# Kernel optimization log

Hardware: AMD Instinct MI355X
Metric: run time of the kernel (lower is better)

Reference implementation:

```python
import jax, jax.numpy as jnp
import numpy as np

B, TM1, E, D = 512, 256, 256, 256  # batch, T-1, encoder_hidden, decoder_hidden


def setup_inputs() -> dict:
    key = jax.random.key(0)
    ks = jax.random.split(key, 10)
    s = 0.05
    return {
        "input_encoded": jax.random.normal(ks[0], (B, TM1, E), dtype=jnp.float32),
        "y_history": jax.random.normal(ks[1], (B, TM1, 1), dtype=jnp.float32),
        # attn_layer: Linear(2D+E -> E), Tanh, Linear(E -> 1)
        "attn_w1": jax.random.normal(ks[2], (E, 2 * D + E), dtype=jnp.float32) * s,
        "attn_b1": jnp.zeros((E,), jnp.float32),
        "attn_w2": jax.random.normal(ks[3], (1, E), dtype=jnp.float32) * s,
        "attn_b2": jnp.zeros((1,), jnp.float32),
        # LSTM cell: input_size=1, hidden=D
        "W_ih": jax.random.normal(ks[4], (4 * D, 1), dtype=jnp.float32) * s,
        "W_hh": jax.random.normal(ks[5], (4 * D, D), dtype=jnp.float32) * s,
        "b_ih": jnp.zeros((4 * D,), jnp.float32),
        "b_hh": jnp.zeros((4 * D,), jnp.float32),
        # fc: Linear(E+1 -> 1), weight init normal_()
        "fc_w": jax.random.normal(ks[6], (1, E + 1), dtype=jnp.float32),
        "fc_b": jnp.zeros((1,), jnp.float32),
        # fc_final: Linear(D+E -> 2) (probabilistic)
        "fcf_w": jax.random.normal(ks[7], (2, D + E), dtype=jnp.float32) * s,
        "fcf_b": jnp.zeros((2,), jnp.float32),
    }


def _forward(input_encoded, y_history, attn_w1, attn_b1, attn_w2, attn_b2,
             W_ih, W_hh, b_ih, b_hh, fc_w, fc_b, fcf_w, fcf_b):
    # Split attn first linear into [hidden|cell] part and encoder part.
    w1_hc = attn_w1[:, : 2 * D]   # (E, 2D)
    w1_enc = attn_w1[:, 2 * D:]   # (E, E)
    # Encoder projection is invariant across timesteps: compute once. (B,TM1,E)
    enc_proj = jnp.einsum("bte,fe->btf", input_encoded, w1_enc) + attn_b1

    def step(carry, y_t):
        h, c, _ = carry  # h,c: (B,D); y_t: (B,1)
        hc = jnp.concatenate([h, c], axis=1)                     # (B, 2D)
        pre = jnp.tanh(enc_proj + (hc @ w1_hc.T)[:, None, :])    # (B, TM1, E)
        scores = jnp.einsum("bte,oe->bto", pre, attn_w2)[..., 0] + attn_b2[0]  # (B, TM1)
        alpha = jax.nn.softmax(scores, axis=1)
        context = jnp.einsum("bt,bte->be", alpha, input_encoded)  # (B, E)
        y_tilde = jnp.concatenate([context, y_t], axis=1) @ fc_w.T + fc_b  # (B,1)
        # LSTM cell (torch gate order: i, f, g, o)
        gates = y_tilde @ W_ih.T + b_ih + h @ W_hh.T + b_hh  # (B, 4D)
        i, f, g, o = jnp.split(gates, 4, axis=1)
        i = jax.nn.sigmoid(i); f = jax.nn.sigmoid(f)
        g = jnp.tanh(g); o = jax.nn.sigmoid(o)
        c_new = f * c + i * g
        h_new = o * jnp.tanh(c_new)
        return (h_new, c_new, context), None

    h0 = jnp.zeros((input_encoded.shape[0], D), input_encoded.dtype)
    c0 = jnp.zeros_like(h0)
    ctx0 = jnp.zeros((input_encoded.shape[0], E), input_encoded.dtype)
    ys = jnp.transpose(y_history, (1, 0, 2))  # (TM1, B, 1)
    (h, c, context), _ = jax.lax.scan(step, (h0, c0, ctx0), ys)
    return jnp.concatenate([h, context], axis=1) @ fcf_w.T + fcf_b  # (B, 2)


def reference(input_encoded, y_history, attn_w1, attn_b1, attn_w2, attn_b2,
              W_ih, W_hh, b_ih, b_hh, fc_w, fc_b, fcf_w, fcf_b):
    return _forward(input_encoded, y_history, attn_w1, attn_b1, attn_w2, attn_b2,
                    W_ih, W_hh, b_ih, b_hh, fc_w, fc_b, fcf_w, fcf_b)
```

## Files before the change

### kernel.cpp

```cpp
#include <hip/hip_runtime.h>
#include <cstdint>
#include <cstddef>


typedef _Float16 half8 __attribute__((ext_vector_type(8)));
typedef _Float16 half4v __attribute__((ext_vector_type(4)));
typedef _Float16 half2v __attribute__((ext_vector_type(2)));

__device__ __forceinline__ float rcpf_(float x) { return __builtin_amdgcn_rcpf(x); }
__device__ __forceinline__ float sigmoidf_(float x) { return rcpf_(1.f + __expf(-x)); }
__device__ __forceinline__ float tanhf_(float x) { return 1.f - 2.f * rcpf_(1.f + __expf(2.f * x)); }

#if defined(__has_builtin)
#if __has_builtin(__builtin_amdgcn_fdot2)
#define HAS_FDOT2 1
#endif
#endif
#ifndef HAS_FDOT2
#define HAS_FDOT2 0
#endif

__device__ __forceinline__ float fdot2_(half2v a, half2v b, float c) {
#if HAS_FDOT2
  return __builtin_amdgcn_fdot2(a, b, c, false);
#else
  return fmaf((float)a[0], (float)b[0], fmaf((float)a[1], (float)b[1], c));
#endif
}

__device__ __forceinline__ float dot8_(half8 w, half8 h, float acc) {
  acc = fdot2_(__builtin_shufflevector(w, w, 0, 1), __builtin_shufflevector(h, h, 0, 1), acc);
  acc = fdot2_(__builtin_shufflevector(w, w, 2, 3), __builtin_shufflevector(h, h, 2, 3), acc);
  acc = fdot2_(__builtin_shufflevector(w, w, 4, 5), __builtin_shufflevector(h, h, 4, 5), acc);
  acc = fdot2_(__builtin_shufflevector(w, w, 6, 7), __builtin_shufflevector(h, h, 6, 7), acc);
  return acc;
}


__global__ void k_prep_wT(const float* __restrict__ w1, float* __restrict__ wT) {
  int id = blockIdx.x * 256 + threadIdx.x;
  int e = id >> 8, f = id & 255;
  wT[id] = w1[f * 768 + 512 + e];
}

__global__ void k_prep_xh(const float* __restrict__ x, _Float16* __restrict__ xh) {
  int id = blockIdx.x * 256 + threadIdx.x;
  float4 v = reinterpret_cast<const float4*>(x)[id];
  half4v h;
  h[0] = (_Float16)v.x; h[1] = (_Float16)v.y; h[2] = (_Float16)v.z; h[3] = (_Float16)v.w;
  reinterpret_cast<half4v*>(xh)[id] = h;
}

__global__ void k_prep_w1hcQ(const float* __restrict__ w1, _Float16* __restrict__ o) {
  int id = blockIdx.x * 256 + threadIdx.x;
  int m = id & 7, lane = (id >> 3) & 511, c = id >> 12;
  int e = lane >> 1, kh = lane & 1;
  o[id] = (_Float16)w1[e * 768 + kh * 256 + c * 8 + m];
}

__global__ void k_prep_whhG(const float* __restrict__ whh, _Float16* __restrict__ o) {
  int id = blockIdx.x * 256 + threadIdx.x;
  int m = id & 7, j = (id >> 3) & 1023, c = id >> 13;
  o[id] = (_Float16)whh[j * 256 + c * 8 + m];
}

__global__ __launch_bounds__(256) void k_xf(const float* __restrict__ x,
                                            const float* __restrict__ fcw,
                                            float* __restrict__ xf) {
  __shared__ float xl[16][256];
  __shared__ float fw[256];
  __shared__ float part[16][17];
  const int tid = threadIdx.x;
  const int m0 = blockIdx.x * 16;
  fw[tid] = fcw[tid];
#pragma unroll
  for (int r = 0; r < 16; ++r) xl[r][tid] = x[(size_t)(m0 + r) * 256 + tid];
  __syncthreads();
  int r = tid >> 4, p = tid & 15;
  float s = 0.f;
#pragma unroll
  for (int u = 0; u < 16; ++u) s = fmaf(xl[r][p * 16 + u], fw[p * 16 + u], s);
  part[r][p] = s;
  __syncthreads();
  if (tid < 16) {
    float t = 0.f;
#pragma unroll
    for (int p2 = 0; p2 < 16; ++p2) t += part[tid][p2];
    xf[m0 + tid] = t;
  }
}

__global__ __launch_bounds__(256) void k_encp(const float* __restrict__ x,
                                              const float* __restrict__ wT,
                                              const float* __restrict__ b1,
                                              _Float16* __restrict__ Ph2) {
  __shared__ __align__(16) float xl[16][256];
  const int tid = threadIdx.x;
  const int m0 = blockIdx.x * 16;
#pragma unroll
  for (int r = 0; r < 16; ++r) xl[r][tid] = x[(size_t)(m0 + r) * 256 + tid];
  __syncthreads();
  float acc[16];
#pragma unroll
  for (int r = 0; r < 16; ++r) acc[r] = 0.f;
  for (int e = 0; e < 256; e += 4) {
    float w0 = wT[(e + 0) * 256 + tid];
    float w1_ = wT[(e + 1) * 256 + tid];
    float w2_ = wT[(e + 2) * 256 + tid];
    float w3_ = wT[(e + 3) * 256 + tid];
#pragma unroll
    for (int r = 0; r < 16; ++r) {
      float4 xv = *reinterpret_cast<const float4*>(&xl[r][e]);
      acc[r] = fmaf(xv.x, w0, acc[r]);
      acc[r] = fmaf(xv.y, w1_, acc[r]);
      acc[r] = fmaf(xv.z, w2_, acc[r]);
      acc[r] = fmaf(xv.w, w3_, acc[r]);
    }
  }
  float bb = b1[tid];
  const int e = tid;
#pragma unroll
  for (int r = 0; r < 16; ++r) {
    int m = m0 + r, b = m >> 8, t = m & 255;
    float p = __expf(2.f * (acc[r] + bb));
    Ph2[((size_t)(b * 32 + (e >> 3)) * 256 + t) * 8 + (e & 7)] = (_Float16)p;
  }
}

#define SC1(pv, c) { \
  float4 qa = q4[2*(c)], wa = w4[2*(c)]; \
  sacc0 = fmaf(wa.x, rcpf_(fmaf((float)pv[0], qa.x, 1.f)), sacc0); \
  sacc1 = fmaf(wa.y, rcpf_(fmaf((float)pv[1], qa.y, 1.f)), sacc1); \
  sacc0 = fmaf(wa.z, rcpf_(fmaf((float)pv[2], qa.z, 1.f)), sacc0); \
  sacc1 = fmaf(wa.w, rcpf_(fmaf((float)pv[3], qa.w, 1.f)), sacc1); \
  float4 qb = q4[2*(c)+1], wb = w4[2*(c)+1]; \
  sacc0 = fmaf(wb.x, rcpf_(fmaf((float)pv[4], qb.x, 1.f)), sacc0); \
  sacc1 = fmaf(wb.y, rcpf_(fmaf((float)pv[5], qb.y, 1.f)), sacc1); \
  sacc0 = fmaf(wb.z, rcpf_(fmaf((float)pv[6], qb.z, 1.f)), sacc0); \
  sacc1 = fmaf(wb.w, rcpf_(fmaf((float)pv[7], qb.w, 1.f)), sacc1); }

__global__ __launch_bounds__(1024, 4) void k_scan(
    const _Float16* __restrict__ Ph2, const _Float16* __restrict__ xh,
    const _Float16* __restrict__ w1hcQ, const _Float16* __restrict__ whhG,
    const float* __restrict__ xf, const float* __restrict__ y_hist,
    const float* __restrict__ w2g, const float* __restrict__ Wih,
    const float* __restrict__ bih, const float* __restrict__ bhh,
    const float* __restrict__ fcw, const float* __restrict__ fcb,
    const float* __restrict__ fcfw, const float* __restrict__ fcfb,
    float* __restrict__ out) {
  __shared__ __align__(16) float hc[2][512];
  __shared__ __align__(16) _Float16 hcH[2][520];
  __shared__ __align__(16) float Qs[2][256];
  __shared__ __align__(16) float spart[2][2][256];
  __shared__ __align__(16) float ealpha[2][256];
  __shared__ __align__(16) float gfull[2][1024];
  __shared__ __align__(16) _Float16 PhL[2][14][256][8];
  __shared__ __align__(16) float w2l[256];
  __shared__ __align__(16) float Wihl[1024];
  __shared__ __align__(16) float bl[1024];
  __shared__ __align__(16) float xfL[2][256];
  __shared__ __align__(16) float yhL[2][256];
  __shared__ float redA[8], redB[8];

  const int tid = threadIdx.x;
  const int b0 = blockIdx.x * 2;
  const int lo = tid & 255;
  const int wv = tid >> 6, lane = tid & 63;

  ((float*)hc)[tid] = 0.f;
  if (tid < 520) {
    hcH[0][tid] = (_Float16)0.f;
    hcH[1][tid] = (_Float16)0.f;
  }
  if (tid < 256) w2l[tid] = w2g[tid];
  Wihl[tid & 1023] = Wih[tid & 1023];
  bl[tid] = bih[tid] + bhh[tid];
  if (tid < 512) {
    int gi = tid >> 8, ti = tid & 255;
    xfL[gi][ti] = xf[(size_t)(b0 + gi) * 256 + ti];
    yhL[gi][ti] = y_hist[(size_t)(b0 + gi) * 256 + ti];
  }
  {
    half8* phl8 = reinterpret_cast<half8*>(&PhL[0][0][0][0]);
    const half8* ph8 = reinterpret_cast<const half8*>(Ph2);
#pragma unroll
    for (int u2 = 0; u2 < 7; ++u2) {
      int slot = u2 * 1024 + tid;
      int g = slot >= 3584;
      int rem = slot - g * 3584;
      int ci = rem >> 8;
      int t = rem & 255;
      int cc = (ci < 7) ? (2 * ci) : (16 + 2 * (ci - 7));
      phl8[slot] = ph8[((size_t)(b0 + g) * 32 + cc) * 256 + t];
    }
  }
  __syncthreads();
  float w2sum = 0.f;
  for (int e2 = 0; e2 < 256; ++e2) w2sum += w2l[e2];
  const float fcb0 = fcb[0];
  const float fcwy = fcw[256];

  const half8* wq2 = reinterpret_cast<const half8*>(w1hcQ) + tid;
  const int khq = tid & 1;
  const int ug = (tid - 512) & 511;
  const half8* wgJ = reinterpret_cast<const half8*>(whhG) + ug;
  const int gs = tid >> 9, eh = (tid >> 8) & 1;
  const half8* prow = reinterpret_cast<const half8*>(Ph2) +
                      ((size_t)((b0 + gs) * 32 + eh * 16)) * 256 + lo;
  const half8* phlR = reinterpret_cast<const half8*>(&PhL[0][0][0][0]) +
                      (gs * 14 + eh * 7) * 256 + lo;
  const int gp = (tid >> 8) & 1;

#pragma unroll 1
  for (int s = 0; s < 256; ++s) {
    if (tid < 512) {
      float a0 = 0.f, a1 = 0.f;
      const half8* hp0 = reinterpret_cast<const half8*>(&hcH[0][khq * 264]);
      const half8* hp1 = reinterpret_cast<const half8*>(&hcH[1][khq * 264]);
#pragma unroll 8
      for (int c = 0; c < 32; ++c) {
        half8 w = wq2[c * 512];
        a0 = dot8_(w, hp0[c], a0);
        a1 = dot8_(w, hp1[c], a1);
      }
      a0 += __shfl_xor(a0, 1);
      a1 += __shfl_xor(a1, 1);
      if (khq == 0) {
        int e = tid >> 1;
        Qs[0][e] = __expf(2.f * a0);
        Qs[1][e] = __expf(2.f * a1);
      }
    } else {
      float ac00 = 0.f, ac01 = 0.f, ac10 = 0.f, ac11 = 0.f;
      const half8* hg0 = reinterpret_cast<const half8*>(&hcH[0][0]);
      const half8* hg1 = reinterpret_cast<const half8*>(&hcH[1][0]);
#pragma unroll 4
      for (int c = 0; c < 32; ++c) {
        half8 h0 = hg0[c];
        half8 h1 = hg1[c];
        half8 w0 = wgJ[c * 1024];
        half8 w1v = wgJ[c * 1024 + 512];
        ac00 = dot8_(w0, h0, ac00);  ac01 = dot8_(w0, h1, ac01);
        ac10 = dot8_(w1v, h0, ac10); ac11 = dot8_(w1v, h1, ac11);
      }
      gfull[0][ug] = ac00;
      gfull[1][ug] = ac01;
      gfull[0][ug + 512] = ac10;
      gfull[1][ug + 512] = ac11;
    }
    __syncthreads();

    float sacc0 = 0.f, sacc1 = 0.f;
    {
      const float4* q4 = reinterpret_cast<const float4*>(&Qs[gs][eh * 128]);
      const float4* w4 = reinterpret_cast<const float4*>(&w2l[eh * 128]);
      half8 s1 = prow[1 * 256];
      half8 s3 = prow[3 * 256];
      half8 s5 = prow[5 * 256];
      half8 s7 = prow[7 * 256];
      half8 s9 = prow[9 * 256];
      half8 s11 = prow[11 * 256];
      half8 s13 = prow[13 * 256];
      half8 s14 = prow[14 * 256];
      half8 s15 = prow[15 * 256];
      { half8 l0 = phlR[0 * 256];  SC1(l0, 0) }
      { half8 l2 = phlR[1 * 256];  SC1(l2, 2) }
      { half8 l4 = phlR[2 * 256];  SC1(l4, 4) }
      { half8 l6 = phlR[3 * 256];  SC1(l6, 6) }
      { half8 l8 = phlR[4 * 256];  SC1(l8, 8) }
      { half8 la = phlR[5 * 256];  SC1(la, 10) }
      { half8 lc = phlR[6 * 256];  SC1(lc, 12) }
      SC1(s1, 1)  SC1(s3, 3)  SC1(s5, 5)  SC1(s7, 7)  SC1(s9, 9)
      SC1(s11, 11) SC1(s13, 13) SC1(s14, 14) SC1(s15, 15)
    }
    spart[eh][gs][lo] = sacc0 + sacc1;
    __syncthreads();

    if (tid < 512) {
      float sc = w2sum - 2.f * (spart[0][gp][lo] + spart[1][gp][lo]);
      float ea = __expf(sc);
      ealpha[gp][lo] = ea;
      float ef = ea * xfL[gp][lo];
      float es = ea;
#pragma unroll
      for (int off = 32; off > 0; off >>= 1) {
        es += __shfl_xor(es, off);
        ef += __shfl_xor(ef, off);
      }
      if (lane == 0) { redA[wv] = es; redB[wv] = ef; }
    }
    __syncthreads();

    if (tid < 512) {
      float es = (gp == 0) ? (redA[0] + redA[1] + redA[2] + redA[3])
                           : (redA[4] + redA[5] + redA[6] + redA[7]);
      float ef = (gp == 0) ? (redB[0] + redB[1] + redB[2] + redB[3])
                           : (redB[4] + redB[5] + redB[6] + redB[7]);
      float yt = ef * rcpf_(es) + fmaf(yhL[gp][s], fcwy, fcb0);
      float gi = fmaf(yt, Wihl[lo], bl[lo]) + gfull[gp][lo];
      float gf = fmaf(yt, Wihl[256 + lo], bl[256 + lo]) + gfull[gp][256 + lo];
      float gc = fmaf(yt, Wihl[512 + lo], bl[512 + lo]) + gfull[gp][512 + lo];
      float go = fmaf(yt, Wihl[768 + lo], bl[768 + lo]) + gfull[gp][768 + lo];
      float iv = sigmoidf_(gi), fv = sigmoidf_(gf), gv = tanhf_(gc), ov = sigmoidf_(go);
      float cold = hc[gp][256 + lo];
      float cn = fmaf(fv, cold, iv * gv);
      float hn = ov * tanhf_(cn);
      hc[gp][lo] = hn;
      hc[gp][256 + lo] = cn;
      hcH[gp][lo] = (_Float16)hn;
      hcH[gp][264 + lo] = (_Float16)cn;
    }
    __syncthreads();
  }

  const float rsA = rcpf_(redA[0] + redA[1] + redA[2] + redA[3]);
  const float rsB = rcpf_(redA[4] + redA[5] + redA[6] + redA[7]);

  float* cpartF = reinterpret_cast<float*>(&PhL[0][0][0][0]);
  {
    const int gc = tid >> 9, t16 = (tid >> 5) & 15, l5 = tid & 31;
    const half8* xrow = reinterpret_cast<const half8*>(xh) +
                        ((size_t)(b0 + gc) * 256 + t16 * 16) * 32 + l5;
    float acx[8];
#pragma unroll
    for (int m = 0; m < 8; ++m) acx[m] = 0.f;
#pragma unroll 4
    for (int it = 0; it < 16; ++it) {
      float al = ealpha[gc][t16 * 16 + it];
      half8 xv = xrow[it * 32];
#pragma unroll
      for (int m = 0; m < 8; ++m) acx[m] = fmaf(al, (float)xv[m], acx[m]);
    }
    float* dst = &cpartF[((gc * 16 + t16) * 256) + l5 * 8];
    *reinterpret_cast<float4*>(dst) = *reinterpret_cast<float4*>(&acx[0]);
    *reinterpret_cast<float4*>(dst + 4) = *reinterpret_cast<float4*>(&acx[4]);
  }
  __syncthreads();

  if (tid < 512) {
    float cv = 0.f;
#pragma unroll
    for (int u = 0; u < 16; ++u) cv += cpartF[((gp * 16 + u) * 256) + lo];
    cv *= (gp == 0) ? rsA : rsB;
    float hval = hc[gp][lo];
    float p0 = hval * fcfw[lo] + cv * fcfw[256 + lo];
    float p1 = hval * fcfw[512 + lo] + cv * fcfw[768 + lo];
#pragma unroll
    for (int off = 32; off > 0; off >>= 1) {
      p0 += __shfl_xor(p0, off);
      p1 += __shfl_xor(p1, off);
    }
    if (lane == 0) { redA[wv] = p0; redB[wv] = p1; }
  }
  __syncthreads();
  if (tid < 4) {
    int g2 = tid >> 1, o = tid & 1;
    const float* r = (o == 0) ? redA : redB;
    float v = fcfb[o] + r[g2 * 4 + 0] + r[g2 * 4 + 1] + r[g2 * 4 + 2] + r[g2 * 4 + 3];
    out[(b0 + g2) * 2 + o] = v;
  }
}

extern "C" void kernel_launch(void* const* d_in, const int* in_sizes, int n_in,
                              void* d_out, int out_size, void* d_ws, size_t ws_size,
                              hipStream_t stream) {
  (void)in_sizes; (void)n_in; (void)out_size; (void)ws_size;
  const float* x    = (const float*)d_in[0];
  const float* yh   = (const float*)d_in[1];
  const float* w1   = (const float*)d_in[2];
  const float* b1   = (const float*)d_in[3];
  const float* w2   = (const float*)d_in[4];
  const float* Wih  = (const float*)d_in[6];
  const float* Whh  = (const float*)d_in[7];
  const float* bih  = (const float*)d_in[8];
  const float* bhh  = (const float*)d_in[9];
  const float* fcw  = (const float*)d_in[10];
  const float* fcb  = (const float*)d_in[11];
  const float* fcfw = (const float*)d_in[12];
  const float* fcfb = (const float*)d_in[13];
  float* out = (float*)d_out;

  char* ws = (char*)d_ws;
  _Float16* Ph2   = (_Float16*)(ws);
  _Float16* xh    = (_Float16*)(ws + (size_t)67108864);
  float*    wT    = (float*)   (ws + (size_t)134217728);
  _Float16* w1hcQ = (_Float16*)(ws + (size_t)134479872);
  _Float16* whhG  = (_Float16*)(ws + (size_t)134742016);
  float*    xf    = (float*)   (ws + (size_t)135266304);

  k_prep_wT   <<<256,   256, 0, stream>>>(w1, wT);
  k_prep_xh   <<<32768, 256, 0, stream>>>(x, xh);
  k_prep_w1hcQ<<<512,   256, 0, stream>>>(w1, w1hcQ);
  k_prep_whhG <<<1024,  256, 0, stream>>>(Whh, whhG);
  k_xf        <<<8192,  256, 0, stream>>>(x, fcw, xf);
  k_encp      <<<8192,  256, 0, stream>>>(x, wT, b1, Ph2);
  k_scan      <<<256,  1024, 0, stream>>>(Ph2, xh, w1hcQ, whhG, xf, yh, w2, Wih,
                                          bih, bhh, fcw, fcb, fcfw, fcfb, out);
}
```

Baseline: 3.662 ms.

## Pair e-halves across adjacent lanes to drop spart barrier; cache half of Ph in LDS

Reassigns the score computation so the two encoder halves for a timestep sit in adjacent lanes, combined with a lane shuffle instead of an LDS partial buffer and an extra __syncthreads. The softmax exp and wave reduction now run across all 1024 threads, so the reduction arrays double to 16 entries. The LDS cache of the projected encoder tile grows from 14 to 16 chunks per batch, so all even chunks come from LDS and only odd chunks from global memory. This removes one block barrier per step and some global loads, at the cost of more LDS, which may reduce occupancy.

```diff
diff --git a/kernel.cpp b/kernel.cpp
--- a/kernel.cpp
+++ b/kernel.cpp
@@ -151,16 +151,15 @@
   __shared__ __align__(16) float hc[2][512];
   __shared__ __align__(16) _Float16 hcH[2][520];
   __shared__ __align__(16) float Qs[2][256];
-  __shared__ __align__(16) float spart[2][2][256];
   __shared__ __align__(16) float ealpha[2][256];
   __shared__ __align__(16) float gfull[2][1024];
-  __shared__ __align__(16) _Float16 PhL[2][14][256][8];
+  __shared__ __align__(16) _Float16 PhL[2][16][256][8];
   __shared__ __align__(16) float w2l[256];
   __shared__ __align__(16) float Wihl[1024];
   __shared__ __align__(16) float bl[1024];
   __shared__ __align__(16) float xfL[2][256];
   __shared__ __align__(16) float yhL[2][256];
-  __shared__ float redA[8], redB[8];
+  __shared__ float redA[16], redB[16];
 
   const int tid = threadIdx.x;
   const int b0 = blockIdx.x * 2;
@@ -184,13 +183,13 @@
     half8* phl8 = reinterpret_cast<half8*>(&PhL[0][0][0][0]);
     const half8* ph8 = reinterpret_cast<const half8*>(Ph2);
 #pragma unroll
-    for (int u2 = 0; u2 < 7; ++u2) {
+    for (int u2 = 0; u2 < 8; ++u2) {
       int slot = u2 * 1024 + tid;
-      int g = slot >= 3584;
-      int rem = slot - g * 3584;
+      int g = slot >= 4096;
+      int rem = slot - g * 4096;
       int ci = rem >> 8;
       int t = rem & 255;
-      int cc = (ci < 7) ? (2 * ci) : (16 + 2 * (ci - 7));
+      int cc = 2 * ci;
       phl8[slot] = ph8[((size_t)(b0 + g) * 32 + cc) * 256 + t];
     }
   }
@@ -204,11 +203,11 @@
   const int khq = tid & 1;
   const int ug = (tid - 512) & 511;
   const half8* wgJ = reinterpret_cast<const half8*>(whhG) + ug;
-  const int gs = tid >> 9, eh = (tid >> 8) & 1;
-  const half8* prow = reinterpret_cast<const half8*>(Ph2) +
-                      ((size_t)((b0 + gs) * 32 + eh * 16)) * 256 + lo;
-  const half8* phlR = reinterpret_cast<const half8*>(&PhL[0][0][0][0]) +
-                      (gs * 14 + eh * 7) * 256 + lo;
+  const int gs = tid >> 9, tp = (tid >> 1) & 255, ehp = tid & 1;
+  const half8* prowP = reinterpret_cast<const half8*>(Ph2) +
+                       ((size_t)((b0 + gs) * 32 + ehp * 16)) * 256 + tp;
+  const half8* phlRP = reinterpret_cast<const half8*>(&PhL[0][0][0][0]) +
+                       (gs * 16 + ehp * 8) * 256 + tp;
   const int gp = (tid >> 8) & 1;
 
 #pragma unroll 1
@@ -250,38 +249,34 @@
     }
     __syncthreads();
 
-    float sacc0 = 0.f, sacc1 = 0.f;
     {
-      const float4* q4 = reinterpret_cast<const float4*>(&Qs[gs][eh * 128]);
-      const float4* w4 = reinterpret_cast<const float4*>(&w2l[eh * 128]);
-      half8 s1 = prow[1 * 256];
-      half8 s3 = prow[3 * 256];
-      half8 s5 = prow[5 * 256];
-      half8 s7 = prow[7 * 256];
-      half8 s9 = prow[9 * 256];
-      half8 s11 = prow[11 * 256];
-      half8 s13 = prow[13 * 256];
-      half8 s14 = prow[14 * 256];
-      half8 s15 = prow[15 * 256];
-      { half8 l0 = phlR[0 * 256];  SC1(l0, 0) }
-      { half8 l2 = phlR[1 * 256];  SC1(l2, 2) }
-      { half8 l4 = phlR[2 * 256];  SC1(l4, 4) }
-      { half8 l6 = phlR[3 * 256];  SC1(l6, 6) }
-      { half8 l8 = phlR[4 * 256];  SC1(l8, 8) }
-      { half8 la = phlR[5 * 256];  SC1(la, 10) }
-      { half8 lc = phlR[6 * 256];  SC1(lc, 12) }
-      SC1(s1, 1)  SC1(s3, 3)  SC1(s5, 5)  SC1(s7, 7)  SC1(s9, 9)
-      SC1(s11, 11) SC1(s13, 13) SC1(s14, 14) SC1(s15, 15)
-    }
-    spart[eh][gs][lo] = sacc0 + sacc1;
-    __syncthreads();
-
-    if (tid < 512) {
-      float sc = w2sum - 2.f * (spart[0][gp][lo] + spart[1][gp][lo]);
-      float ea = __expf(sc);
-      ealpha[gp][lo] = ea;
-      float ef = ea * xfL[gp][lo];
-      float es = ea;
+      float sacc0 = 0.f, sacc1 = 0.f;
+      const float4* q4 = reinterpret_cast<const float4*>(&Qs[gs][ehp * 128]);
+      const float4* w4 = reinterpret_cast<const float4*>(&w2l[ehp * 128]);
+      half8 s1 = prowP[1 * 256];
+      half8 s3 = prowP[3 * 256];
+      half8 s5 = prowP[5 * 256];
+      half8 s7 = prowP[7 * 256];
+      half8 s9 = prowP[9 * 256];
+      half8 s11 = prowP[11 * 256];
+      half8 s13 = prowP[13 * 256];
+      half8 s15 = prowP[15 * 256];
+      { half8 l = phlRP[0 * 256]; SC1(l, 0) }
+      { half8 l = phlRP[1 * 256]; SC1(l, 2) }
+      { half8 l = phlRP[2 * 256]; SC1(l, 4) }
+      { half8 l = phlRP[3 * 256]; SC1(l, 6) }
+      { half8 l = phlRP[4 * 256]; SC1(l, 8) }
+      { half8 l = phlRP[5 * 256]; SC1(l, 10) }
+      { half8 l = phlRP[6 * 256]; SC1(l, 12) }
+      { half8 l = phlRP[7 * 256]; SC1(l, 14) }
+      SC1(s1, 1)  SC1(s3, 3)  SC1(s5, 5)  SC1(s7, 7)
+      SC1(s9, 9)  SC1(s11, 11) SC1(s13, 13) SC1(s15, 15)
+      float sacc = sacc0 + sacc1;
+      sacc += __shfl_xor(sacc, 1);
+      float ea = __expf(w2sum - 2.f * sacc);
+      if (ehp == 0) ealpha[gs][tp] = ea;
+      float es = (ehp == 0) ? ea : 0.f;
+      float ef = es * xfL[gs][tp];
 #pragma unroll
       for (int off = 32; off > 0; off >>= 1) {
         es += __shfl_xor(es, off);
@@ -292,10 +287,11 @@
     __syncthreads();
 
     if (tid < 512) {
-      float es = (gp == 0) ? (redA[0] + redA[1] + redA[2] + redA[3])
-                           : (redA[4] + redA[5] + redA[6] + redA[7]);
-      float ef = (gp == 0) ? (redB[0] + redB[1] + redB[2] + redB[3])
-                           : (redB[4] + redB[5] + redB[6] + redB[7]);
+      const int rb = gp * 8;
+      float es = redA[rb + 0] + redA[rb + 1] + redA[rb + 2] + redA[rb + 3] +
+                 redA[rb + 4] + redA[rb + 5] + redA[rb + 6] + redA[rb + 7];
+      float ef = redB[rb + 0] + redB[rb + 1] + redB[rb + 2] + redB[rb + 3] +
+                 redB[rb + 4] + redB[rb + 5] + redB[rb + 6] + redB[rb + 7];
       float yt = ef * rcpf_(es) + fmaf(yhL[gp][s], fcwy, fcb0);
       float gi = fmaf(yt, Wihl[lo], bl[lo]) + gfull[gp][lo];
       float gf = fmaf(yt, Wihl[256 + lo], bl[256 + lo]) + gfull[gp][256 + lo];
@@ -313,8 +309,10 @@
     __syncthreads();
   }
 
-  const float rsA = rcpf_(redA[0] + redA[1] + redA[2] + redA[3]);
-  const float rsB = rcpf_(redA[4] + redA[5] + redA[6] + redA[7]);
+  const float rsA = rcpf_(redA[0] + redA[1] + redA[2] + redA[3] +
+                          redA[4] + redA[5] + redA[6] + redA[7]);
+  const float rsB = rcpf_(redA[8] + redA[9] + redA[10] + redA[11] +
+                          redA[12] + redA[13] + redA[14] + redA[15]);
 
   float* cpartF = reinterpret_cast<float*>(&PhL[0][0][0][0]);
   {
```

Result: no change. 3.653 ms (-0.2%).
